# Optimization experiments

Hardware: AMD Instinct MI355X
Metric: run time of the kernel (lower is better)

The kernel has to match this reference:

```python
import jax, jax.numpy as jnp
import numpy as np

NQ, NS, QN, SN = 10000, 500, 4, 10   # num_question, num_skill, q/s neighbor sizes
B, S, D = 32, 200, 128               # batch, seq_len, emb_dim
HOPS = 3


def setup_inputs() -> dict:
    key = jax.random.key(0)
    ks = iter(jax.random.split(key, 40))

    def nrm(shape, scale=0.05):
        return jax.random.normal(next(ks), shape, dtype=jnp.float32) * scale

    return {
        "question": jax.random.randint(next(ks), (B, S), 0, NQ),
        "response": jax.random.randint(next(ks), (B, S), 0, 2),
        "mask": jnp.ones((B, S), dtype=jnp.int32),
        "q_neighbors": jax.random.randint(next(ks), (NQ, QN), 0, NS),  # question -> skill ids
        "s_neighbors": jax.random.randint(next(ks), (NS, SN), 0, NQ),  # skill -> question ids
        "qs_skills": jax.random.randint(next(ks), (NQ, 4), 0, NS),     # related skills per question
        "emb_q": nrm((NQ, D), 1.0),
        "emb_s": nrm((NS, D), 1.0),
        "emb_r": nrm((2, D), 1.0),
        "W_ih": nrm((2 * D, 4 * D)), "b_ih": nrm((4 * D,)), "b_hh": nrm((4 * D,)),
        "ft_W": nrm((D, D)), "ft_b": nrm((D,)),
        "agg_W": nrm((HOPS, D, D)), "agg_b": nrm((HOPS, D)),
        "last_W": nrm((D, D)), "last_b": nrm((D,)),
        "q_W": nrm((D, D)), "q_b": nrm((D,)),
        "k_W": nrm((D, D)), "k_b": nrm((D,)),
        "w_W": nrm((2 * D,)), "w_b": nrm(()),
    }


def reference(question, response, mask, q_neighbors, s_neighbors, qs_skills,
              emb_q, emb_s, emb_r, W_ih, b_ih, b_hh, ft_W, ft_b,
              agg_W, agg_b, last_W, last_b, q_W, q_b, k_W, k_b, w_W, w_b):
    # ---- multi-hop GNN aggregation for every (b, t) question (mask == 1 everywhere) ----
    q_flat = question.reshape(-1)              # [B*S]
    lvl1 = q_neighbors[q_flat]                 # [N, QN]            skill ids
    lvl2 = s_neighbors[lvl1]                   # [N, QN, SN]        question ids
    lvl3 = q_neighbors[lvl2]                   # [N, QN, SN, QN]    skill ids
    embs = [emb_q[q_flat], emb_s[lvl1], emb_q[lvl2], emb_s[lvl3]]
    for i in range(HOPS):
        embs = [jnp.tanh((embs[j] + embs[j + 1].mean(axis=-2)) @ agg_W[j] + agg_b[j])
                for j in range(HOPS - i)]
    agg_emb = jnp.tanh(embs[0] @ last_W + last_b).reshape(B, S, D)

    # ---- per-step input + zero-state LSTMCell (source calls lstm_cell without hx) ----
    q_trans = jax.nn.relu(agg_emb @ ft_W + ft_b)
    x = jnp.concatenate([q_trans, emb_r[response]], axis=-1)   # [B, S, 2D]
    gates = x @ W_ih + b_ih + b_hh                             # h_prev = 0, c_prev = 0
    i_g, f_g, g_g, o_g = jnp.split(gates, 4, axis=-1)
    c = jax.nn.sigmoid(i_g) * jnp.tanh(g_g)
    h = jax.nn.sigmoid(o_g) * jnp.tanh(c)                      # [B, S, D]
    states = h[:, :S - 1]                                      # state written at step t

    # ---- soft-recap attention prediction for q_next = question[:, t+1] ----
    q_next = question[:, 1:]                                   # [B, T], T = S-1
    qs = jnp.concatenate([emb_q[q_next][:, :, None, :], emb_s[qs_skills[q_next]]], axis=2)  # [B,T,5,D]

    inner = jnp.einsum('bnd,btmd->btnm', states, qs)           # state/qs inner products
    a_state = (states @ q_W + q_b) @ w_W[:D]                   # [B, N]  MLP_query on states
    a_qs = (qs @ k_W + k_b) @ w_W[D:]                          # [B, T, 5] MLP_key on qs
    logits = a_state[:, None, :, None] + a_qs[:, :, None, :] + w_b  # [B, T, N, 5]

    t_idx = jnp.arange(S - 1)
    valid = t_idx[None, :] <= t_idx[:, None]                   # [T, N]: states 0..t visible at t
    logits = jnp.where(valid[None, :, :, None], logits, -jnp.inf)
    alpha = jax.nn.softmax(logits.reshape(B, S - 1, -1), axis=-1).reshape(logits.shape)
    pred = jnp.sum(alpha * jax.nn.sigmoid(inner), axis=(2, 3))  # [B, T]

    return jnp.zeros((B, S), jnp.float32).at[:, 1:].set(pred)
```

## Files before the change

kernel.cpp:

```cpp
#include <hip/hip_runtime.h>

typedef unsigned short u16;
typedef unsigned int   u32;

#define NQd 10000
#define NSd 500
#define Bd  32
#define Sd  200
#define Td  199
#define Dd  128
#define NR  6368
#define PB  208

typedef __attribute__((ext_vector_type(8))) short bf16x8;
typedef __attribute__((ext_vector_type(4))) float f32x4;

__device__ __forceinline__ float sigf(float x) {
  return __builtin_amdgcn_rcpf(1.f + __expf(-x));
}
__device__ __forceinline__ float tanh_f(float x) {
  float ax = fminf(fabsf(x), 15.f);
  float e = __expf(2.f * ax);
  float r = 1.f - 2.f * __builtin_amdgcn_rcpf(e + 1.f);
  return copysignf(r, x);
}
__device__ __forceinline__ float bf2f(u16 u) { return __uint_as_float(((u32)u) << 16); }
__device__ __forceinline__ u16 f2bf(float f) {
  u32 b = __float_as_uint(f);
  b += 0x7FFFu + ((b >> 16) & 1u);
  return (u16)(b >> 16);
}
__device__ __forceinline__ void unp2(u32 u, float &a, float &b) {
  a = __uint_as_float(u << 16);
  b = __uint_as_float(u & 0xffff0000u);
}
__device__ __forceinline__ void unpack16(uint4 a0, uint4 a1, float* f) {
  unp2(a0.x, f[0], f[1]);  unp2(a0.y, f[2], f[3]);
  unp2(a0.z, f[4], f[5]);  unp2(a0.w, f[6], f[7]);
  unp2(a1.x, f[8], f[9]);  unp2(a1.y, f[10], f[11]);
  unp2(a1.z, f[12], f[13]); unp2(a1.w, f[14], f[15]);
}

struct Args {
  const int *question, *response, *q_nb, *s_nb, *qs_sk;
  const float *emb_q, *emb_s, *emb_r;
  const float *W_ih, *b_ih, *b_hh, *ft_W, *ft_b, *agg_W, *agg_b, *last_W, *last_b;
  const float *q_W, *q_b, *k_W, *k_b, *w_W;
  u16 *tabA, *tabB, *tabs1, *tabs2, *states, *embq_bf, *embs_bf, *wts, *wiht;
  float *a_state, *qw, *kw, *scal, *er_part, *ev, *invZ, *pred_acc, *pm;
  int *qid_map, *resp_map;
};

#define SMEM_U16 21760

__device__ __forceinline__ void mfma_accum(const u16* Al, const u16* Wl,
                                           int l15, int quad, int cw, f32x4 acc[2][2])
{
#pragma unroll
  for (int kc = 0; kc < 4; ++kc) {
    const int ko = kc * 32 + quad * 8;
    bf16x8 af[2], bfv[2];
    af[0]  = *(const bf16x8*)&Al[l15 * 136 + ko];
    af[1]  = *(const bf16x8*)&Al[(16 + l15) * 136 + ko];
    bfv[0] = *(const bf16x8*)&Wl[(cw + l15) * 136 + ko];
    bfv[1] = *(const bf16x8*)&Wl[(cw + 16 + l15) * 136 + ko];
#pragma unroll
    for (int mt = 0; mt < 2; ++mt)
#pragma unroll
      for (int nt = 0; nt < 2; ++nt)
        acc[mt][nt] = __builtin_amdgcn_mfma_f32_16x16x32_bf16(af[mt], bfv[nt], acc[mt][nt], 0, 0, 0);
  }
}

__device__ __forceinline__ void zero_acc(f32x4 acc[2][2]) {
#pragma unroll
  for (int x = 0; x < 2; ++x)
#pragma unroll
    for (int y = 0; y < 2; ++y) acc[x][y] = (f32x4){0.f, 0.f, 0.f, 0.f};
}

__device__ __forceinline__ void stage_A(const u16* Atab, const u16* Btab,
                                        const int* nbr, int K, int tile0, int rows,
                                        int tid, u16* Al)
{
  int r = tid & 31, k0 = (tid >> 5) * 16;
  int row = tile0 + r; if (row >= rows) row = rows - 1;
  const u16* ap = Atab + (long)row * 128 + k0;
  if (K == 0) {
    *(uint4*)&Al[r * 136 + k0]     = *(const uint4*)ap;
    *(uint4*)&Al[r * 136 + k0 + 8] = *(const uint4*)(ap + 8);
  } else {
    float f[16];
    unpack16(*(const uint4*)ap, *(const uint4*)(ap + 8), f);
    float s[16];
#pragma unroll
    for (int q = 0; q < 16; ++q) s[q] = 0.f;
    for (int l = 0; l < K; ++l) {
      int id = nbr[(long)row * K + l];
      const u16* np = Btab + (long)id * 128 + k0;
      float g[16];
      unpack16(*(const uint4*)np, *(const uint4*)(np + 8), g);
#pragma unroll
      for (int q = 0; q < 16; ++q) s[q] += g[q];
    }
    float inv = 1.f / (float)K;
#pragma unroll
    for (int q = 0; q < 16; ++q) f[q] += s[q] * inv;
    u32 p[8];
#pragma unroll
    for (int q = 0; q < 8; ++q)
      p[q] = (u32)f2bf(f[2 * q]) | ((u32)f2bf(f[2 * q + 1]) << 16);
    *(uint4*)&Al[r * 136 + k0]     = make_uint4(p[0], p[1], p[2], p[3]);
    *(uint4*)&Al[r * 136 + k0 + 8] = make_uint4(p[4], p[5], p[6], p[7]);
  }
}

__device__ __forceinline__ void update_A(const u16* Btab, const int* nbr,
                                         int tile0, int rows, int tid, u16* Al)
{
  int r = tid & 31, k0 = (tid >> 5) * 16;
  int row = tile0 + r; if (row >= rows) row = rows - 1;
  float f[16];
  unpack16(*(const uint4*)&Al[r * 136 + k0], *(const uint4*)&Al[r * 136 + k0 + 8], f);
  float s[16];
#pragma unroll
  for (int q = 0; q < 16; ++q) s[q] = 0.f;
#pragma unroll
  for (int l = 0; l < 4; ++l) {
    int id = nbr[(long)row * 4 + l];
    const u16* np = Btab + (long)id * 128 + k0;
    float g[16];
    unpack16(*(const uint4*)np, *(const uint4*)(np + 8), g);
#pragma unroll
    for (int q = 0; q < 16; ++q) s[q] += g[q];
  }
#pragma unroll
  for (int q = 0; q < 16; ++q) f[q] += s[q] * 0.25f;
  u32 p[8];
#pragma unroll
  for (int q = 0; q < 8; ++q)
    p[q] = (u32)f2bf(f[2 * q]) | ((u32)f2bf(f[2 * q + 1]) << 16);
  *(uint4*)&Al[r * 136 + k0]     = make_uint4(p[0], p[1], p[2], p[3]);
  *(uint4*)&Al[r * 136 + k0 + 8] = make_uint4(p[4], p[5], p[6], p[7]);
}

__device__ __forceinline__ void stage_W(const u16* Wt, int tid, u16* Wl)
{
  for (int i = tid; i < 2048; i += 256) {
    int col = i >> 4, seg = i & 15;
    *(uint4*)&Wl[col * 136 + seg * 8] = *(const uint4*)&Wt[(long)col * 128 + seg * 8];
  }
}

__device__ __forceinline__ void epi_tanh_global(const f32x4 acc[2][2], const float* cbias,
                                                u16* out, int rows, int tile0,
                                                int l15, int quad, int cw)
{
#pragma unroll
  for (int nt = 0; nt < 2; ++nt) {
    int col = cw + nt * 16 + l15;
    float cb = cbias[col];
#pragma unroll
    for (int mt = 0; mt < 2; ++mt) {
      int rbase = tile0 + mt * 16 + quad * 4;
#pragma unroll
      for (int i = 0; i < 4; ++i) {
        int row = rbase + i;
        if (row >= rows) continue;
        out[(long)row * 128 + col] = f2bf(tanh_f(acc[mt][nt][i] + cb));
      }
    }
  }
}

__device__ __forceinline__ void epi_tanh_lds(const f32x4 acc[2][2], const float* cbias,
                                             u16* Al, int l15, int quad, int cw)
{
#pragma unroll
  for (int nt = 0; nt < 2; ++nt) {
    int col = cw + nt * 16 + l15;
    float cb = cbias[col];
#pragma unroll
    for (int mt = 0; mt < 2; ++mt)
#pragma unroll
      for (int i = 0; i < 4; ++i) {
        int rL = mt * 16 + quad * 4 + i;
        Al[rL * 136 + col] = f2bf(tanh_f(acc[mt][nt][i] + cb));
      }
  }
}

__device__ __forceinline__ void gemm_tile(
    const u16* __restrict__ Atab, const u16* __restrict__ Btab,
    const int* __restrict__ nbr, int K,
    const u16* __restrict__ Wt, const float* __restrict__ cbias,
    u16* __restrict__ out, int rows, int tile0, int tid, u16* smem)
{
  u16* Wl = smem;
  u16* Al = smem + 17408;
  stage_W(Wt, tid, Wl);
  stage_A(Atab, Btab, nbr, K, tile0, rows, tid, Al);
  __syncthreads();
  const int lane = tid & 63, wv = tid >> 6;
  const int l15 = lane & 15, quad = lane >> 4, cw = wv * 32;
  f32x4 acc[2][2];
  zero_acc(acc);
  mfma_accum(Al, Wl, l15, quad, cw, acc);
  epi_tanh_global(acc, cbias, out, rows, tile0, l15, quad, cw);
}

__global__ __launch_bounds__(256) void prep_all(Args a)
{
  const int T = gridDim.x * 256;
  for (int i = blockIdx.x * 256 + threadIdx.x; i < 491106; i += T) {
    if (i < 320000) {
      float4 v = *(const float4*)&a.emb_q[(long)i * 4];
      ((uint2*)a.embq_bf)[i] = make_uint2(
          (u32)f2bf(v.x) | ((u32)f2bf(v.y) << 16),
          (u32)f2bf(v.z) | ((u32)f2bf(v.w) << 16));
    } else if (i < 336000) {
      int c = i - 320000;
      float4 v = *(const float4*)&a.emb_s[(long)c * 4];
      ((uint2*)a.embs_bf)[c] = make_uint2(
          (u32)f2bf(v.x) | ((u32)f2bf(v.y) << 16),
          (u32)f2bf(v.z) | ((u32)f2bf(v.w) << 16));
    } else if (i < 417920) {
      int e = i - 336000;
      int seg = e >> 14, r = e & 16383;
      int col = r >> 7, k = r & 127;
      const float* src = (seg < 3) ? (a.agg_W + seg * 16384)
                                   : (seg == 3 ? a.last_W : a.ft_W);
      a.wts[e] = f2bf(src[k * 128 + col]);
    } else if (i < 483456) {
      int e = i - 417920;
      int col = e >> 7, k = e & 127;
      a.wiht[e] = f2bf(a.W_ih[k * 512 + col]);
    } else if (i < 489824) {
      int j = i - 483456;
      int b = j / Td, s = j - b * Td;
      a.qid_map[j]  = a.question[b * Sd + s];
      a.resp_map[j] = a.response[b * Sd + s];
    } else {
      int s = i - 489824;
      if (s < 128) {
        float acc = 0;
        for (int e = 0; e < 128; ++e) acc += a.q_W[s * 128 + e] * a.w_W[e];
        a.qw[s] = acc;
      } else if (s < 256) {
        int d = s - 128; float acc = 0;
        for (int e = 0; e < 128; ++e) acc += a.k_W[d * 128 + e] * a.w_W[128 + e];
        a.kw[d] = acc;
      } else if (s == 256) {
        float acc = 0;
        for (int e = 0; e < 128; ++e) acc += a.q_b[e] * a.w_W[e];
        a.scal[0] = acc;
      } else if (s == 257) {
        float acc = 0;
        for (int e = 0; e < 128; ++e) acc += a.k_b[e] * a.w_W[128 + e];
        a.scal[1] = acc;
      } else {
        int e2 = s - 258, rr = e2 >> 9, col = e2 & 511;
        float acc = a.b_ih[col] + a.b_hh[col];
        for (int d = 0; d < 128; ++d) acc += a.emb_r[rr * Dd + d] * a.W_ih[(128 + d) * 512 + col];
        a.er_part[rr * 512 + col] = acc;
      }
    }
  }
}

__global__ __launch_bounds__(256) void level1m(Args a)
{
  __shared__ __align__(16) u16 smem[SMEM_U16];
  const int i = blockIdx.x, tid = threadIdx.x;
  if (i >= 313) {
    gemm_tile(a.embs_bf, a.embq_bf, a.s_nb, 10, a.wts + 16384,
              a.agg_b + 128, a.tabs1, NSd, (i - 313) * 32, tid, smem);
    return;
  }
  u16* Wl = smem;
  u16* Al = smem + 17408;
  const int tile0 = i * 32;
  const int lane = tid & 63, wv = tid >> 6;
  const int l15 = lane & 15, quad = lane >> 4, cw = wv * 32;
  f32x4 acc[2][2];
  stage_W(a.wts + 2 * 16384, tid, Wl);
  stage_A(a.embq_bf, a.embs_bf, a.q_nb, 4, tile0, NQd, tid, Al);
  __syncthreads();
  zero_acc(acc);
  mfma_accum(Al, Wl, l15, quad, cw, acc);
  epi_tanh_global(acc, a.agg_b + 256, a.tabA, NQd, tile0, l15, quad, cw);
  __syncthreads();
  stage_W(a.wts, tid, Wl);
  __syncthreads();
  zero_acc(acc);
  mfma_accum(Al, Wl, l15, quad, cw, acc);
  epi_tanh_global(acc, a.agg_b, a.tabB, NQd, tile0, l15, quad, cw);
}

__global__ __launch_bounds__(256) void g1k(Args a)
{
  __shared__ __align__(16) u16 smem[SMEM_U16];
  const int tid = threadIdx.x;
  gemm_tile(a.tabs1, a.tabA, a.s_nb, 10, a.wts + 16384,
            a.agg_b + 128, a.tabs2, NSd, blockIdx.x * 32, tid, smem);
}

__global__ __launch_bounds__(256) void chain4(Args a)
{
  __shared__ __align__(16) u16 smem[SMEM_U16];
  u16* Wl = smem;
  u16* Al = smem + 17408;
  const int tid = threadIdx.x;
  const int tile0 = blockIdx.x * 32;
  const int lane = tid & 63, wv = tid >> 6;
  const int l15 = lane & 15, quad = lane >> 4, cw = wv * 32;
  f32x4 acc[2][2];

  stage_W(a.wts, tid, Wl);
  stage_A(a.tabB, a.tabs1, a.q_nb, 4, tile0, NQd, tid, Al);
  __syncthreads();
  zero_acc(acc);
  mfma_accum(Al, Wl, l15, quad, cw, acc);
  __syncthreads();
  epi_tanh_lds(acc, a.agg_b, Al, l15, quad, cw);
  __syncthreads();

  update_A(a.tabs2, a.q_nb, tile0, NQd, tid, Al);
  __syncthreads();
  zero_acc(acc);
  mfma_accum(Al, Wl, l15, quad, cw, acc);
  __syncthreads();
  epi_tanh_lds(acc, a.agg_b, Al, l15, quad, cw);
  stage_W(a.wts + 3 * 16384, tid, Wl);
  __syncthreads();

  zero_acc(acc);
  mfma_accum(Al, Wl, l15, quad, cw, acc);
  __syncthreads();
  epi_tanh_lds(acc, a.last_b, Al, l15, quad, cw);
  stage_W(a.wts + 4 * 16384, tid, Wl);
  __syncthreads();

  zero_acc(acc);
  mfma_accum(Al, Wl, l15, quad, cw, acc);
#pragma unroll
  for (int nt = 0; nt < 2; ++nt) {
    int col = cw + nt * 16 + l15;
    float cb = a.ft_b[col];
#pragma unroll
    for (int mt = 0; mt < 2; ++mt) {
      int rbase = tile0 + mt * 16 + quad * 4;
#pragma unroll
      for (int i = 0; i < 4; ++i) {
        int row = rbase + i;
        if (row >= NQd) continue;
        a.tabA[(long)row * 128 + col] = f2bf(fmaxf(acc[mt][nt][i] + cb, 0.f));
      }
    }
  }
}

__global__ __launch_bounds__(256) void gates_k(Args a)
{
  __shared__ __align__(16) u16 smem[SMEM_U16];
  u16* Wl = smem;
  u16* Al = smem + 17408;
  const int tid = threadIdx.x;
  const int tile0 = blockIdx.x * 32;
  {
    int r = tid & 31, k0 = (tid >> 5) * 16;
    int row = tile0 + r;
    int arow = a.qid_map[row];
    const u16* ap = a.tabA + (long)arow * 128 + k0;
    *(uint4*)&Al[r * 136 + k0]     = *(const uint4*)ap;
    *(uint4*)&Al[r * 136 + k0 + 8] = *(const uint4*)(ap + 8);
  }
  const int lane = tid & 63, wv = tid >> 6;
  const int l15 = lane & 15, quad = lane >> 4, cw = wv * 32;
  f32x4 acc[3][2][2];
  const int goff[3] = {0, 256, 384};
#pragma unroll
  for (int p = 0; p < 3; ++p) {
    __syncthreads();
    stage_W(a.wiht + (long)goff[p] * 128, tid, Wl);
    __syncthreads();
    zero_acc(acc[p]);
    mfma_accum(Al, Wl, l15, quad, cw, acc[p]);
  }
  __syncthreads();
  float* hb = (float*)Wl;
#pragma unroll
  for (int nt = 0; nt < 2; ++nt) {
    int colL = cw + nt * 16 + l15;
#pragma unroll
    for (int mt = 0; mt < 2; ++mt) {
#pragma unroll
      for (int i = 0; i < 4; ++i) {
        int rL = mt * 16 + quad * 4 + i;
        int row = tile0 + rL;
        const float* rb = a.er_part + (long)a.resp_map[row] * 512;
        float iv = acc[0][mt][nt][i] + rb[colL];
        float gv = acc[1][mt][nt][i] + rb[256 + colL];
        float ov = acc[2][mt][nt][i] + rb[384 + colL];
        float c = sigf(iv) * tanh_f(gv);
        float h = sigf(ov) * tanh_f(c);
        a.states[(long)row * 128 + colL] = f2bf(h);
        hb[rL * 132 + colL] = h;
      }
    }
  }
  __syncthreads();
#pragma unroll
  for (int rr = 0; rr < 8; ++rr) {
    int rL = wv * 8 + rr;
    float p = hb[rL * 132 + lane] * a.qw[lane] + hb[rL * 132 + 64 + lane] * a.qw[64 + lane];
#pragma unroll
    for (int off = 32; off > 0; off >>= 1) p += __shfl_xor(p, off);
    if (lane == 0) a.a_state[tile0 + rL] = p + a.scal[0];
  }
}

__global__ __launch_bounds__(256) void bprep(Args a)
{
  __shared__ float red[256];
  __shared__ float evl[256];
  __shared__ float kwl[128];
  const int b = blockIdx.x, tid = threadIdx.x;
  if (tid < 128) kwl[tid] = a.kw[tid];
  float v = (tid < Td) ? a.a_state[b * Td + tid] : -1e30f;
  red[tid] = v; __syncthreads();
  for (int s = 128; s > 0; s >>= 1) { if (tid < s) red[tid] = fmaxf(red[tid], red[tid + s]); __syncthreads(); }
  float gmax = red[0];
  float e = (tid < Td) ? __expf(v - gmax) : 0.f;
  evl[tid] = e;
  if (tid < Td) { a.ev[b * PB + tid] = e; a.pred_acc[b * PB + tid] = 0.f; }
  __syncthreads();
  for (int off = 1; off < 256; off <<= 1) {
    float add = (tid >= off) ? evl[tid - off] : 0.f;
    __syncthreads();
    evl[tid] += add;
    __syncthreads();
  }
  if (tid < Td) {
    a.invZ[b * PB + tid] = 1.f / evl[tid];
    int qn = a.question[b * Sd + tid + 1];
    float am[5];
#pragma unroll
    for (int m = 0; m < 5; ++m) {
      const u16* src = (m == 0) ? a.embq_bf + (long)qn * 128
                                : a.embs_bf + (long)a.qs_sk[qn * 4 + (m - 1)] * 128;
      float s = 0.f;
      for (int k = 0; k < 128; k += 8) {
        uint4 u = *(const uint4*)&src[k];
        float f[8];
        unp2(u.x, f[0], f[1]); unp2(u.y, f[2], f[3]);
        unp2(u.z, f[4], f[5]); unp2(u.w, f[6], f[7]);
#pragma unroll
        for (int q = 0; q < 8; ++q) s = fmaf(f[q], kwl[k + q], s);
      }
      am[m] = s + a.scal[1];
    }
    float mx = am[0];
#pragma unroll
    for (int m = 1; m < 5; ++m) mx = fmaxf(mx, am[m]);
    float ex[5], z = 0.f;
#pragma unroll
    for (int m = 0; m < 5; ++m) { ex[m] = __expf(am[m] - mx); z += ex[m]; }
    float iz = 1.f / z;
#pragma unroll
    for (int m = 0; m < 5; ++m) a.pm[((long)b * PB + tid) * 5 + m] = ex[m] * iz;
  }
}

__global__ __launch_bounds__(256) void gk_pred(Args a)
{
  const int n0 = blockIdx.x * 32;
  const int c0 = blockIdx.y * 128;
  const int b  = blockIdx.z;
  int c_hi = c0 + 127; if (c_hi > 994) c_hi = 994;
  const int tmax = c_hi / 5, tmin = c0 / 5;
  if (n0 > tmax) return;

  __shared__ __align__(16) u16 smem[SMEM_U16];
  __shared__ float predl[32];
  u16* Ql = smem;
  u16* Sl = smem + 17408;
  const int tid = threadIdx.x;
  if (tid < 32) predl[tid] = 0.f;
  {
    int r = tid & 31, k0 = (tid >> 5) * 16;
    int n = n0 + r; if (n > 198) n = 198;
    const u16* sp = a.states + ((long)b * Td + n) * 128 + k0;
    *(uint4*)&Sl[r * 136 + k0]     = *(const uint4*)sp;
    *(uint4*)&Sl[r * 136 + k0 + 8] = *(const uint4*)(sp + 8);
  }
  {
    int j = tid >> 1, k0 = (tid & 1) * 64;
    int col = c0 + j;
    uint4* dst = (uint4*)&Ql[j * 136 + k0];
    if (col < 995) {
      int t = col / 5, m = col - t * 5;
      int qn = a.question[b * Sd + t + 1];
      const u16* src = (m == 0) ? a.embq_bf + (long)qn * 128
                                : a.embs_bf + (long)a.qs_sk[qn * 4 + (m - 1)] * 128;
      src += k0;
#pragma unroll
      for (int q = 0; q < 8; ++q) dst[q] = ((const uint4*)src)[q];
    } else {
      uint4 z = make_uint4(0, 0, 0, 0);
#pragma unroll
      for (int q = 0; q < 8; ++q) dst[q] = z;
    }
  }
  __syncthreads();
  const int lane = tid & 63, wv = tid >> 6;
  const int l15 = lane & 15, quad = lane >> 4, cw = wv * 32;
  f32x4 acc[2][2];
  zero_acc(acc);
  mfma_accum(Sl, Ql, l15, quad, cw, acc);

#pragma unroll
  for (int nt = 0; nt < 2; ++nt) {
    int col = c0 + cw + nt * 16 + l15;
    if (col >= 995) continue;
    int t = col / 5, m = col - t * 5;
    float pmv = a.pm[((long)b * PB + t) * 5 + m];
    float part = 0.f;
#pragma unroll
    for (int mt = 0; mt < 2; ++mt) {
      int nb = n0 + mt * 16 + quad * 4;
      if (nb > t) continue;
      float4 ev4 = *(const float4*)&a.ev[b * PB + nb];
      float evv[4] = {ev4.x, ev4.y, ev4.z, ev4.w};
#pragma unroll
      for (int i = 0; i < 4; ++i) {
        int n = nb + i;
        if (n > t || n > 198) continue;
        part += evv[i] * sigf(acc[mt][nt][i]);
      }
    }
    part *= pmv;
    if (part != 0.f) atomicAdd(&predl[t - tmin], part);
  }
  __syncthreads();
  const int tcnt = tmax - tmin + 1;
  if (tid < tcnt) {
    float pv = predl[tid];
    if (pv != 0.f) atomicAdd(&a.pred_acc[b * PB + tmin + tid], pv);
  }
}

__global__ __launch_bounds__(256) void finalize(Args a, float* __restrict__ out)
{
  int i = blockIdx.x * 256 + threadIdx.x;
  if (i >= Bd * Sd) return;
  int b = i / Sd, s = i - b * Sd;
  out[i] = (s == 0) ? 0.f : a.pred_acc[b * PB + s - 1] * a.invZ[b * PB + s - 1];
}

extern "C" void kernel_launch(void* const* d_in, const int* in_sizes, int n_in,
                              void* d_out, int out_size, void* d_ws, size_t ws_size,
                              hipStream_t stream)
{
  Args a;
  a.question = (const int*)d_in[0];
  a.response = (const int*)d_in[1];
  a.q_nb     = (const int*)d_in[3];
  a.s_nb     = (const int*)d_in[4];
  a.qs_sk    = (const int*)d_in[5];
  a.emb_q    = (const float*)d_in[6];
  a.emb_s    = (const float*)d_in[7];
  a.emb_r    = (const float*)d_in[8];
  a.W_ih     = (const float*)d_in[9];
  a.b_ih     = (const float*)d_in[10];
  a.b_hh     = (const float*)d_in[11];
  a.ft_W     = (const float*)d_in[12];
  a.ft_b     = (const float*)d_in[13];
  a.agg_W    = (const float*)d_in[14];
  a.agg_b    = (const float*)d_in[15];
  a.last_W   = (const float*)d_in[16];
  a.last_b   = (const float*)d_in[17];
  a.q_W      = (const float*)d_in[18];
  a.q_b      = (const float*)d_in[19];
  a.k_W      = (const float*)d_in[20];
  a.k_b      = (const float*)d_in[21];
  a.w_W      = (const float*)d_in[22];

  u16* wsu = (u16*)d_ws;
  const long NT = 1280000, ST = 64000, RT = (long)NR * Dd;
  a.tabA  = wsu;
  a.tabB  = a.tabA + NT;
  a.tabs1 = a.tabB + NT;
  a.tabs2 = a.tabs1 + ST;
  a.states  = a.tabs2 + ST;
  a.embq_bf = a.states + RT;
  a.embs_bf = a.embq_bf + NT;
  a.wts     = a.embs_bf + ST;
  a.wiht    = a.wts + 5 * 16384;
  float* fp = (float*)(a.wiht + 65536);
  a.a_state = fp;
  a.qw      = fp + 6368;
  a.kw      = fp + 6496;
  a.scal    = fp + 6624;
  a.er_part = fp + 6640;
  a.ev       = fp + 7664;
  a.invZ     = a.ev + 32 * PB;
  a.pred_acc = a.invZ + 32 * PB;
  a.pm       = a.pred_acc + 32 * PB;
  a.qid_map  = (int*)(a.pm + 32 * PB * 5);
  a.resp_map = a.qid_map + NR;

  float* out = (float*)d_out;

  prep_all<<<640, 256, 0, stream>>>(a);
  level1m<<<329, 256, 0, stream>>>(a);
  g1k<<<16, 256, 0, stream>>>(a);
  chain4<<<313, 256, 0, stream>>>(a);
  gates_k<<<199, 256, 0, stream>>>(a);
  bprep<<<Bd, 256, 0, stream>>>(a);
  gk_pred<<<dim3(7, 8, Bd), 256, 0, stream>>>(a);
  finalize<<<25, 256, 0, stream>>>(a, out);
}
```

Baseline: 197.5 us.

## Load weight fragments into registers directly and move key-softmax into level1m

Weight tiles are now read straight from global memory into per-wave register fragments (WF) instead of being staged through shared memory. This removes several LDS staging passes and barriers in level1m, g1k, chain4 and gates_k, and shrinks shared memory per block, which may raise occupancy. The per-question key softmax (pm) is moved out of the 32-block bprep kernel into 25 extra blocks of level1m so it runs spread across many blocks earlier. The trade-off is higher register pressure from holding up to three weight fragments per wave, plus redundant global weight reads per block.

```diff
diff --git a/kernel.cpp b/kernel.cpp
--- a/kernel.cpp
+++ b/kernel.cpp
@@ -51,32 +51,37 @@
   int *qid_map, *resp_map;
 };
 
-#define SMEM_U16 21760
-
-__device__ __forceinline__ void mfma_accum(const u16* Al, const u16* Wl,
-                                           int l15, int quad, int cw, f32x4 acc[2][2])
+struct WF { bf16x8 v[2][4]; };
+
+__device__ __forceinline__ void load_WF(const u16* Wt, int l15, int quad, int cw, WF& w)
+{
+#pragma unroll
+  for (int nt = 0; nt < 2; ++nt)
+#pragma unroll
+    for (int kc = 0; kc < 4; ++kc)
+      w.v[nt][kc] = *(const bf16x8*)&Wt[(long)(cw + nt * 16 + l15) * 128 + kc * 32 + quad * 8];
+}
+
+__device__ __forceinline__ void zero_acc(f32x4 acc[2][2]) {
+#pragma unroll
+  for (int x = 0; x < 2; ++x)
+#pragma unroll
+    for (int y = 0; y < 2; ++y) acc[x][y] = (f32x4){0.f, 0.f, 0.f, 0.f};
+}
+
+__device__ __forceinline__ void mfma_WF(const u16* Al, const WF& w,
+                                        int l15, int quad, f32x4 acc[2][2])
 {
 #pragma unroll
   for (int kc = 0; kc < 4; ++kc) {
     const int ko = kc * 32 + quad * 8;
-    bf16x8 af[2], bfv[2];
-    af[0]  = *(const bf16x8*)&Al[l15 * 136 + ko];
-    af[1]  = *(const bf16x8*)&Al[(16 + l15) * 136 + ko];
-    bfv[0] = *(const bf16x8*)&Wl[(cw + l15) * 136 + ko];
-    bfv[1] = *(const bf16x8*)&Wl[(cw + 16 + l15) * 136 + ko];
-#pragma unroll
-    for (int mt = 0; mt < 2; ++mt)
-#pragma unroll
-      for (int nt = 0; nt < 2; ++nt)
-        acc[mt][nt] = __builtin_amdgcn_mfma_f32_16x16x32_bf16(af[mt], bfv[nt], acc[mt][nt], 0, 0, 0);
-  }
-}
-
-__device__ __forceinline__ void zero_acc(f32x4 acc[2][2]) {
-#pragma unroll
-  for (int x = 0; x < 2; ++x)
-#pragma unroll
-    for (int y = 0; y < 2; ++y) acc[x][y] = (f32x4){0.f, 0.f, 0.f, 0.f};
+    bf16x8 a0 = *(const bf16x8*)&Al[l15 * 136 + ko];
+    bf16x8 a1 = *(const bf16x8*)&Al[(16 + l15) * 136 + ko];
+    acc[0][0] = __builtin_amdgcn_mfma_f32_16x16x32_bf16(a0, w.v[0][kc], acc[0][0], 0, 0, 0);
+    acc[0][1] = __builtin_amdgcn_mfma_f32_16x16x32_bf16(a0, w.v[1][kc], acc[0][1], 0, 0, 0);
+    acc[1][0] = __builtin_amdgcn_mfma_f32_16x16x32_bf16(a1, w.v[0][kc], acc[1][0], 0, 0, 0);
+    acc[1][1] = __builtin_amdgcn_mfma_f32_16x16x32_bf16(a1, w.v[1][kc], acc[1][1], 0, 0, 0);
+  }
 }
 
 __device__ __forceinline__ void stage_A(const u16* Atab, const u16* Btab,
@@ -144,14 +149,6 @@
   *(uint4*)&Al[r * 136 + k0 + 8] = make_uint4(p[4], p[5], p[6], p[7]);
 }
 
-__device__ __forceinline__ void stage_W(const u16* Wt, int tid, u16* Wl)
-{
-  for (int i = tid; i < 2048; i += 256) {
-    int col = i >> 4, seg = i & 15;
-    *(uint4*)&Wl[col * 136 + seg * 8] = *(const uint4*)&Wt[(long)col * 128 + seg * 8];
-  }
-}
-
 __device__ __forceinline__ void epi_tanh_global(const f32x4 acc[2][2], const float* cbias,
                                                 u16* out, int rows, int tile0,
                                                 int l15, int quad, int cw)
@@ -188,25 +185,6 @@
         Al[rL * 136 + col] = f2bf(tanh_f(acc[mt][nt][i] + cb));
       }
   }
-}
-
-__device__ __forceinline__ void gemm_tile(
-    const u16* __restrict__ Atab, const u16* __restrict__ Btab,
-    const int* __restrict__ nbr, int K,
-    const u16* __restrict__ Wt, const float* __restrict__ cbias,
-    u16* __restrict__ out, int rows, int tile0, int tid, u16* smem)
-{
-  u16* Wl = smem;
-  u16* Al = smem + 17408;
-  stage_W(Wt, tid, Wl);
-  stage_A(Atab, Btab, nbr, K, tile0, rows, tid, Al);
-  __syncthreads();
-  const int lane = tid & 63, wv = tid >> 6;
-  const int l15 = lane & 15, quad = lane >> 4, cw = wv * 32;
-  f32x4 acc[2][2];
-  zero_acc(acc);
-  mfma_accum(Al, Wl, l15, quad, cw, acc);
-  epi_tanh_global(acc, cbias, out, rows, tile0, l15, quad, cw);
 }
 
 __global__ __launch_bounds__(256) void prep_all(Args a)
@@ -270,79 +248,117 @@
 
 __global__ __launch_bounds__(256) void level1m(Args a)
 {
-  __shared__ __align__(16) u16 smem[SMEM_U16];
+  __shared__ __align__(16) u16 Al[32 * 136];
   const int i = blockIdx.x, tid = threadIdx.x;
-  if (i >= 313) {
-    gemm_tile(a.embs_bf, a.embq_bf, a.s_nb, 10, a.wts + 16384,
-              a.agg_b + 128, a.tabs1, NSd, (i - 313) * 32, tid, smem);
-    return;
-  }
-  u16* Wl = smem;
-  u16* Al = smem + 17408;
-  const int tile0 = i * 32;
   const int lane = tid & 63, wv = tid >> 6;
   const int l15 = lane & 15, quad = lane >> 4, cw = wv * 32;
+
+  if (i >= 329) {
+    int item = (i - 329) * 256 + tid;
+    if (item >= NR) return;
+    int b = item / Td, t = item - b * Td;
+    int qn = a.question[b * Sd + t + 1];
+    float am[5];
+#pragma unroll
+    for (int m = 0; m < 5; ++m) {
+      const u16* src = (m == 0) ? a.embq_bf + (long)qn * 128
+                                : a.embs_bf + (long)a.qs_sk[qn * 4 + (m - 1)] * 128;
+      float s = 0.f;
+      for (int k = 0; k < 128; k += 8) {
+        uint4 u = *(const uint4*)&src[k];
+        float f[8];
+        unp2(u.x, f[0], f[1]); unp2(u.y, f[2], f[3]);
+        unp2(u.z, f[4], f[5]); unp2(u.w, f[6], f[7]);
+#pragma unroll
+        for (int q = 0; q < 8; ++q) s = fmaf(f[q], a.kw[k + q], s);
+      }
+      am[m] = s + a.scal[1];
+    }
+    float mx = am[0];
+#pragma unroll
+    for (int m = 1; m < 5; ++m) mx = fmaxf(mx, am[m]);
+    float ex[5], z = 0.f;
+#pragma unroll
+    for (int m = 0; m < 5; ++m) { ex[m] = __expf(am[m] - mx); z += ex[m]; }
+    float iz = __builtin_amdgcn_rcpf(z);
+#pragma unroll
+    for (int m = 0; m < 5; ++m) a.pm[((long)b * PB + t) * 5 + m] = ex[m] * iz;
+    return;
+  }
+
   f32x4 acc[2][2];
-  stage_W(a.wts + 2 * 16384, tid, Wl);
+  if (i >= 313) {
+    const int tile0 = (i - 313) * 32;
+    WF w1; load_WF(a.wts + 16384, l15, quad, cw, w1);
+    stage_A(a.embs_bf, a.embq_bf, a.s_nb, 10, tile0, NSd, tid, Al);
+    __syncthreads();
+    zero_acc(acc);
+    mfma_WF(Al, w1, l15, quad, acc);
+    epi_tanh_global(acc, a.agg_b + 128, a.tabs1, NSd, tile0, l15, quad, cw);
+    return;
+  }
+  const int tile0 = i * 32;
+  WF w2, w0;
+  load_WF(a.wts + 2 * 16384, l15, quad, cw, w2);
+  load_WF(a.wts, l15, quad, cw, w0);
   stage_A(a.embq_bf, a.embs_bf, a.q_nb, 4, tile0, NQd, tid, Al);
   __syncthreads();
   zero_acc(acc);
-  mfma_accum(Al, Wl, l15, quad, cw, acc);
+  mfma_WF(Al, w2, l15, quad, acc);
   epi_tanh_global(acc, a.agg_b + 256, a.tabA, NQd, tile0, l15, quad, cw);
-  __syncthreads();
-  stage_W(a.wts, tid, Wl);
-  __syncthreads();
-  zero_acc(acc);
-  mfma_accum(Al, Wl, l15, quad, cw, acc);
+  zero_acc(acc);
+  mfma_WF(Al, w0, l15, quad, acc);
   epi_tanh_global(acc, a.agg_b, a.tabB, NQd, tile0, l15, quad, cw);
 }
 
 __global__ __launch_bounds__(256) void g1k(Args a)
 {
-  __shared__ __align__(16) u16 smem[SMEM_U16];
-  const int tid = threadIdx.x;
-  gemm_tile(a.tabs1, a.tabA, a.s_nb, 10, a.wts + 16384,
-            a.agg_b + 128, a.tabs2, NSd, blockIdx.x * 32, tid, smem);
-}
-
-__global__ __launch_bounds__(256) void chain4(Args a)
-{
-  __shared__ __align__(16) u16 smem[SMEM_U16];
-  u16* Wl = smem;
-  u16* Al = smem + 17408;
-  const int tid = threadIdx.x;
-  const int tile0 = blockIdx.x * 32;
+  __shared__ __align__(16) u16 Al[32 * 136];
+  const int tid = threadIdx.x, tile0 = blockIdx.x * 32;
   const int lane = tid & 63, wv = tid >> 6;
   const int l15 = lane & 15, quad = lane >> 4, cw = wv * 32;
+  WF w1; load_WF(a.wts + 16384, l15, quad, cw, w1);
+  stage_A(a.tabs1, a.tabA, a.s_nb, 10, tile0, NSd, tid, Al);
+  __syncthreads();
   f32x4 acc[2][2];
-
-  stage_W(a.wts, tid, Wl);
+  zero_acc(acc);
+  mfma_WF(Al, w1, l15, quad, acc);
+  epi_tanh_global(acc, a.agg_b + 128, a.tabs2, NSd, tile0, l15, quad, cw);
+}
+
+__global__ __launch_bounds__(256) void chain4(Args a)
+{
+  __shared__ __align__(16) u16 Al[32 * 136];
+  const int tid = threadIdx.x, tile0 = blockIdx.x * 32;
+  const int lane = tid & 63, wv = tid >> 6;
+  const int l15 = lane & 15, quad = lane >> 4, cw = wv * 32;
+  WF w0, w3, w4;
+  load_WF(a.wts, l15, quad, cw, w0);
+  load_WF(a.wts + 3 * 16384, l15, quad, cw, w3);
+  load_WF(a.wts + 4 * 16384, l15, quad, cw, w4);
+  f32x4 acc[2][2];
+
   stage_A(a.tabB, a.tabs1, a.q_nb, 4, tile0, NQd, tid, Al);
   __syncthreads();
   zero_acc(acc);
-  mfma_accum(Al, Wl, l15, quad, cw, acc);
+  mfma_WF(Al, w0, l15, quad, acc);
   __syncthreads();
   epi_tanh_lds(acc, a.agg_b, Al, l15, quad, cw);
   __syncthreads();
-
   update_A(a.tabs2, a.q_nb, tile0, NQd, tid, Al);
   __syncthreads();
   zero_acc(acc);
-  mfma_accum(Al, Wl, l15, quad, cw, acc);
+  mfma_WF(Al, w0, l15, quad, acc);
   __syncthreads();
   epi_tanh_lds(acc, a.agg_b, Al, l15, quad, cw);
-  stage_W(a.wts + 3 * 16384, tid, Wl);
-  __syncthreads();
-
-  zero_acc(acc);
-  mfma_accum(Al, Wl, l15, quad, cw, acc);
+  __syncthreads();
+  zero_acc(acc);
+  mfma_WF(Al, w3, l15, quad, acc);
   __syncthreads();
   epi_tanh_lds(acc, a.last_b, Al, l15, quad, cw);
-  stage_W(a.wts + 4 * 16384, tid, Wl);
-  __syncthreads();
-
-  zero_acc(acc);
-  mfma_accum(Al, Wl, l15, quad, cw, acc);
+  __syncthreads();
+  zero_acc(acc);
+  mfma_WF(Al, w4, l15, quad, acc);
 #pragma unroll
   for (int nt = 0; nt < 2; ++nt) {
     int col = cw + nt * 16 + l15;
@@ -362,11 +378,15 @@
 
 __global__ __launch_bounds__(256) void gates_k(Args a)
 {
-  __shared__ __align__(16) u16 smem[SMEM_U16];
-  u16* Wl = smem;
-  u16* Al = smem + 17408;
-  const int tid = threadIdx.x;
-  const int tile0 = blockIdx.x * 32;
+  __shared__ __align__(16) u16 Al[32 * 136];
+  __shared__ float hb[32 * 132];
+  const int tid = threadIdx.x, tile0 = blockIdx.x * 32;
+  const int lane = tid & 63, wv = tid >> 6;
+  const int l15 = lane & 15, quad = lane >> 4, cw = wv * 32;
+  WF wg0, wg1, wg2;
+  load_WF(a.wiht, l15, quad, cw, wg0);
+  load_WF(a.wiht + (long)256 * 128, l15, quad, cw, wg1);
+  load_WF(a.wiht + (long)384 * 128, l15, quad, cw, wg2);
   {
     int r = tid & 31, k0 = (tid >> 5) * 16;
     int row = tile0 + r;
@@ -375,20 +395,11 @@
     *(uint4*)&Al[r * 136 + k0]     = *(const uint4*)ap;
     *(uint4*)&Al[r * 136 + k0 + 8] = *(const uint4*)(ap + 8);
   }
-  const int lane = tid & 63, wv = tid >> 6;
-  const int l15 = lane & 15, quad = lane >> 4, cw = wv * 32;
+  __syncthreads();
   f32x4 acc[3][2][2];
-  const int goff[3] = {0, 256, 384};
-#pragma unroll
-  for (int p = 0; p < 3; ++p) {
-    __syncthreads();
-    stage_W(a.wiht + (long)goff[p] * 128, tid, Wl);
-    __syncthreads();
-    zero_acc(acc[p]);
-    mfma_accum(Al, Wl, l15, quad, cw, acc[p]);
-  }
-  __syncthreads();
-  float* hb = (float*)Wl;
+  zero_acc(acc[0]); mfma_WF(Al, wg0, l15, quad, acc[0]);
+  zero_acc(acc[1]); mfma_WF(Al, wg1, l15, quad, acc[1]);
+  zero_acc(acc[2]); mfma_WF(Al, wg2, l15, quad, acc[2]);
 #pragma unroll
   for (int nt = 0; nt < 2; ++nt) {
     int colL = cw + nt * 16 + l15;
@@ -424,9 +435,7 @@
 {
   __shared__ float red[256];
   __shared__ float evl[256];
-  __shared__ float kwl[128];
   const int b = blockIdx.x, tid = threadIdx.x;
-  if (tid < 128) kwl[tid] = a.kw[tid];
   float v = (tid < Td) ? a.a_state[b * Td + tid] : -1e30f;
   red[tid] = v; __syncthreads();
   for (int s = 128; s > 0; s >>= 1) { if (tid < s) red[tid] = fmaxf(red[tid], red[tid + s]); __syncthreads(); }
@@ -441,35 +450,7 @@
     evl[tid] += add;
     __syncthreads();
   }
-  if (tid < Td) {
-    a.invZ[b * PB + tid] = 1.f / evl[tid];
-    int qn = a.question[b * Sd + tid + 1];
-    float am[5];
-#pragma unroll
-    for (int m = 0; m < 5; ++m) {
-      const u16* src = (m == 0) ? a.embq_bf + (long)qn * 128
-                                : a.embs_bf + (long)a.qs_sk[qn * 4 + (m - 1)] * 128;
-      float s = 0.f;
-      for (int k = 0; k < 128; k += 8) {
-        uint4 u = *(const uint4*)&src[k];
-        float f[8];
-        unp2(u.x, f[0], f[1]); unp2(u.y, f[2], f[3]);
-        unp2(u.z, f[4], f[5]); unp2(u.w, f[6], f[7]);
-#pragma unroll
-        for (int q = 0; q < 8; ++q) s = fmaf(f[q], kwl[k + q], s);
-      }
-      am[m] = s + a.scal[1];
-    }
-    float mx = am[0];
-#pragma unroll
-    for (int m = 1; m < 5; ++m) mx = fmaxf(mx, am[m]);
-    float ex[5], z = 0.f;
-#pragma unroll
-    for (int m = 0; m < 5; ++m) { ex[m] = __expf(am[m] - mx); z += ex[m]; }
-    float iz = 1.f / z;
-#pragma unroll
-    for (int m = 0; m < 5; ++m) a.pm[((long)b * PB + tid) * 5 + m] = ex[m] * iz;
-  }
+  if (tid < Td) a.invZ[b * PB + tid] = 1.f / evl[tid];
 }
 
 __global__ __launch_bounds__(256) void gk_pred(Args a)
@@ -481,7 +462,7 @@
   const int tmax = c_hi / 5, tmin = c0 / 5;
   if (n0 > tmax) return;
 
-  __shared__ __align__(16) u16 smem[SMEM_U16];
+  __shared__ __align__(16) u16 smem[21760];
   __shared__ float predl[32];
   u16* Ql = smem;
   u16* Sl = smem + 17408;
@@ -517,7 +498,20 @@
   const int l15 = lane & 15, quad = lane >> 4, cw = wv * 32;
   f32x4 acc[2][2];
   zero_acc(acc);
-  mfma_accum(Sl, Ql, l15, quad, cw, acc);
+#pragma unroll
+  for (int kc = 0; kc < 4; ++kc) {
+    const int ko = kc * 32 + quad * 8;
+    bf16x8 af[2], bfv[2];
+    af[0]  = *(const bf16x8*)&Sl[l15 * 136 + ko];
+    af[1]  = *(const bf16x8*)&Sl[(16 + l15) * 136 + ko];
+    bfv[0] = *(const bf16x8*)&Ql[(cw + l15) * 136 + ko];
+    bfv[1] = *(const bf16x8*)&Ql[(cw + 16 + l15) * 136 + ko];
+#pragma unroll
+    for (int mt = 0; mt < 2; ++mt)
+#pragma unroll
+      for (int nt = 0; nt < 2; ++nt)
+        acc[mt][nt] = __builtin_amdgcn_mfma_f32_16x16x32_bf16(af[mt], bfv[nt], acc[mt][nt], 0, 0, 0);
+  }
 
 #pragma unroll
   for (int nt = 0; nt < 2; ++nt) {
@@ -613,7 +607,7 @@
   float* out = (float*)d_out;
 
   prep_all<<<640, 256, 0, stream>>>(a);
-  level1m<<<329, 256, 0, stream>>>(a);
+  level1m<<<354, 256, 0, stream>>>(a);
   g1k<<<16, 256, 0, stream>>>(a);
   chain4<<<313, 256, 0, stream>>>(a);
   gates_k<<<199, 256, 0, stream>>>(a);
```

Result: no change. 196.6 us (-0.4%).
